# Performance work log

Measured on AMD Instinct MI355X. Metric: run time of the kernel, lower is better.

Reference implementation:

```python
import jax, jax.numpy as jnp
import numpy as np

# ---- module hyperparameters ----
B, L, F = 128, 720, 128
SEG = 24            # segment_length
NSEG = L // SEG     # 30 input segments
WIN = 15            # window_size
NPRED = 96 // SEG   # 4 prediction segments
D = 128             # encode_dim
H = 512             # hidden_dim
DECAY = 0.9
C = 1.0             # curvature
EPS = 1e-6
MAXN = 1.0 - 1e-5   # max radius of Poincare ball (c=1)
SQC = 1.0           # sqrt(C)

# ---- Poincare-ball manifold ops ----
def _sqnorm(x):
    return jnp.sum(x * x, axis=-1, keepdims=True)

def _norm(x):
    return jnp.sqrt(jnp.maximum(_sqnorm(x), EPS * EPS))

def _project(x):
    n = _norm(x)
    return jnp.where(n > MAXN, x * (MAXN / n), x)

def _artanh(x):
    return jnp.arctanh(jnp.clip(x, -1.0 + 1e-7, 1.0 - 1e-7))

def mobius_add(x, y):
    xy = jnp.sum(x * y, axis=-1, keepdims=True)
    x2, y2 = _sqnorm(x), _sqnorm(y)
    num = (1.0 + 2.0 * C * xy + C * y2) * x + (1.0 - C * x2) * y
    den = 1.0 + 2.0 * C * xy + C * C * x2 * y2
    return num / jnp.maximum(den, EPS)

def expmap0(v):
    n = _norm(v)
    return _project(jnp.tanh(SQC * n) * v / (SQC * n))

def logmap0(y):
    n = _norm(y)
    return _artanh(SQC * n) * y / (SQC * n)

def expmap(x, v):
    lam = 2.0 / jnp.maximum(1.0 - C * _sqnorm(x), EPS)
    n = _norm(v)
    second = jnp.tanh(SQC * lam * n / 2.0) * v / (SQC * n)
    return _project(mobius_add(x, second))

def logmap(x, y):
    d = mobius_add(-x, y)
    n = _norm(d)
    lam = 2.0 / jnp.maximum(1.0 - C * _sqnorm(x), EPS)
    return (2.0 / (SQC * lam)) * _artanh(SQC * n) * d / n


def setup_inputs() -> dict:
    key = jax.random.key(0)
    ks = jax.random.split(key, 12)
    s = 0.05
    return {
        'trend':           0.5 * jax.random.normal(ks[0], (B, L, F), jnp.float32),
        'seasonal_coarse': 0.5 * jax.random.normal(ks[1], (B, L, F), jnp.float32),
        'seasonal_fine':   0.5 * jax.random.normal(ks[2], (B, L, F), jnp.float32),
        'residual':        0.5 * jax.random.normal(ks[3], (B, L, F), jnp.float32),
        'W_t': s * jax.random.normal(ks[4], (SEG, D), jnp.float32), 'b_t': jnp.zeros((D,), jnp.float32),
        'W_c': s * jax.random.normal(ks[5], (SEG, D), jnp.float32), 'b_c': jnp.zeros((D,), jnp.float32),
        'W_f': s * jax.random.normal(ks[6], (SEG, D), jnp.float32), 'b_f': jnp.zeros((D,), jnp.float32),
        'W_r': s * jax.random.normal(ks[7], (SEG, D), jnp.float32), 'b_r': jnp.zeros((D,), jnp.float32),
        'alpha': jnp.array([0.5], jnp.float32),
        'W1': s * jax.random.normal(ks[8], (D, H), jnp.float32), 'b1': jnp.zeros((H,), jnp.float32),
        'W2': s * jax.random.normal(ks[9], (H, SEG), jnp.float32), 'b2': jnp.zeros((SEG,), jnp.float32),
    }


def reference(trend, seasonal_coarse, seasonal_fine, residual,
              W_t, b_t, W_c, b_c, W_f, b_f, W_r, b_r,
              alpha, W1, b1, W2, b2):
    b, l, f = trend.shape

    def collapse(x):  # [B,L,F] -> [B*F, NSEG, SEG]
        return x.transpose(0, 2, 1).reshape(b * f, NSEG, SEG)

    t_s, c_s, f_s, r_s = map(collapse, (trend, seasonal_coarse, seasonal_fine, residual))

    # per-segment tangent encoding (channel-independent, shared params)
    tan = (jnp.einsum('bns,sd->bnd', t_s, W_t) + b_t
           + jnp.einsum('bns,sd->bnd', c_s, W_c) + b_c
           + jnp.einsum('bns,sd->bnd', f_s, W_f) + b_f
           + jnp.einsum('bns,sd->bnd', r_s, W_r) + b_r)
    z = expmap0(tan)                     # [BF, NSEG, D] on the ball
    z_cur = z[:, -WIN:, :]

    idx = jnp.arange(WIN - 1, dtype=jnp.float32)
    w = DECAY ** (WIN - 2 - idx)
    w = w / w.sum()

    preds, latents = [], []
    for _ in range(NPRED):
        z_last = z_cur[:, -1]
        vel = logmap(z_cur[:, :-1], z_cur[:, 1:])
        avg_v = jnp.sum(vel * w[None, :, None], axis=1)    # [BF, D]
        z_next = expmap(z_last, alpha * avg_v)             # dynamics step
        latents.append(z_next)
        # reconstruction head: logmap0 -> MLP -> segment
        t0 = logmap0(z_next)
        seg = jax.nn.relu(t0 @ W1 + b1) @ W2 + b2          # [BF, SEG]
        preds.append(seg)
        z_cur = jnp.concatenate([z_cur[:, 1:], z_next[:, None]], axis=1)

    p = jnp.stack(preds, axis=1).reshape(b * f, NPRED * SEG)
    predictions = p.reshape(b, f, NPRED * SEG).transpose(0, 2, 1)  # [B, pred_len, F]
    return predictions
```

## Files before the change

### kernel.cpp

```cpp
#include <hip/hip_runtime.h>
#include <hip/hip_bf16.h>

namespace {
constexpr int kL = 720, kF = 128;
constexpr int kWin = 15;
constexpr float kEps = 1e-6f;
constexpr float kMaxN = 1.0f - 1e-5f;
constexpr int kT0off = 360;
constexpr int ZTR = 132;
constexpr int AROW = 104;
constexpr size_t kOffT0   = 0;
constexpr size_t kOffW1   = 16777216;
constexpr size_t kOffW2   = kOffW1 + 131072;
constexpr size_t kOffBt   = kOffW2 + 32768;
constexpr size_t kOffBsum = kOffBt + 73728;
constexpr size_t kOffHid  = 17825792;
constexpr size_t kWsSplit = kOffHid + 67108864;
}

typedef float f32x4 __attribute__((ext_vector_type(4)));
typedef short s16x8 __attribute__((ext_vector_type(8)));

__device__ __forceinline__ float rcp_f(float x) { return __builtin_amdgcn_rcpf(x); }
__device__ __forceinline__ float sqrt_f(float x) { return __builtin_amdgcn_sqrtf(x); }
__device__ __forceinline__ float tanh_f(float x) {
  float t = __builtin_amdgcn_exp2f(x * -2.8853900817779268f);
  return (1.0f - t) * rcp_f(1.0f + t);
}
__device__ __forceinline__ float artanh_f(float n) {
  float nc = fminf(n, 1.0f - 1e-7f);
  return 0.34657359027997264f * __builtin_amdgcn_logf((1.0f + nc) * rcp_f(1.0f - nc));
}

template<int CTRL>
__device__ __forceinline__ float dpp_add(float v) {
  int mv = __builtin_amdgcn_update_dpp(0, __float_as_int(v), CTRL, 0xF, 0xF, false);
  return v + __int_as_float(mv);
}
__device__ __forceinline__ float sum16(float v) {
  v = dpp_add<0xB1>(v);
  v = dpp_add<0x4E>(v);
  v = dpp_add<0x141>(v);
  v = dpp_add<0x128>(v);
  return v;
}
__device__ __forceinline__ float sum64(float v) {
  v = sum16(v);
  v += __shfl_xor(v, 16);
  v += __shfl_xor(v, 32);
  return v;
}
__device__ __forceinline__ float rlane(float v, int i) {
  return __int_as_float(__builtin_amdgcn_readlane(__float_as_int(v), i));
}

extern "C" __global__ __launch_bounds__(256)
void mwhf_prep(const float* __restrict__ W1, const float* __restrict__ W2,
               const float* __restrict__ W_t, const float* __restrict__ W_c,
               const float* __restrict__ W_f, const float* __restrict__ W_r,
               const float* __restrict__ b_t, const float* __restrict__ b_c,
               const float* __restrict__ b_f, const float* __restrict__ b_r,
               __hip_bfloat16* __restrict__ W1bf, __hip_bfloat16* __restrict__ W2bf,
               __hip_bfloat16* __restrict__ BtH, __hip_bfloat16* __restrict__ BtM,
               __hip_bfloat16* __restrict__ BtL, float* __restrict__ bsum)
{
  const int b = blockIdx.x, tid = threadIdx.x;
  if (b < 64) {
    const int n0 = b * 8;
    for (int e = tid; e < 1024; e += 256) {
      int n_l = e & 7, k = e >> 3;
      W1bf[(size_t)(n0 + n_l) * 128 + k] = __float2bfloat16(W1[(size_t)k * 512 + n0 + n_l]);
    }
  } else if (b < 68) {
    const int k0 = (b - 64) * 128;
    for (int e = tid; e < 4096; e += 256) {
      int p = e >> 7, k_l = e & 127;
      float v = (p < 24) ? W2[(size_t)(k0 + k_l) * 24 + p] : 0.0f;
      W2bf[(size_t)p * 512 + k0 + k_l] = __float2bfloat16(v);
    }
  } else if (b < 72) {
    const int st = b - 68;
    const float* src = (st == 0) ? W_t : (st == 1) ? W_c : (st == 2) ? W_f : W_r;
    for (int e = tid; e < 3072; e += 256) {
      int s = e >> 7, d = e & 127;
      float x = src[e];
      __hip_bfloat16 h = __float2bfloat16(x);
      float r1 = x - __bfloat162float(h);
      __hip_bfloat16 m = __float2bfloat16(r1);
      float r2 = r1 - __bfloat162float(m);
      const int o = d * 96 + st * 24 + s;
      BtH[o] = h;
      BtM[o] = m;
      BtL[o] = __float2bfloat16(r2);
    }
  } else {
    if (tid < 128) bsum[tid] = b_t[tid] + b_c[tid] + b_f[tid] + b_r[tid];
  }
}

extern "C" __global__ __launch_bounds__(256, 4)
void mwhf_k1(const float* __restrict__ trend,
             const float* __restrict__ seas_c,
             const float* __restrict__ seas_f,
             const float* __restrict__ resid,
             const __hip_bfloat16* __restrict__ BtH,
             const __hip_bfloat16* __restrict__ BtM,
             const __hip_bfloat16* __restrict__ BtL,
             const float* __restrict__ bsum,
             const float* __restrict__ alpha,
             __hip_bfloat16* __restrict__ t0_out)
{
  __shared__ __align__(16) char smem_raw[3 * 64 * AROW * 2];
  __shared__ float z2s[80];
  __shared__ float pds[80];

  float* ublk = (float*)smem_raw;
  __hip_bfloat16* Ah = (__hip_bfloat16*)smem_raw;
  __hip_bfloat16* Am = Ah + 64 * AROW;
  __hip_bfloat16* Al = Am + 64 * AROW;

  const int tid = threadIdx.x;
  const int bix = blockIdx.x;
  const int bb = (bix & 7) * 16 + (bix >> 8);
  const int f0 = ((bix >> 3) & 31) * 4;
  const int row0 = bb * 128 + f0;

  for (int e = tid; e < 192; e += 256) {
    int rr = e / 48, cc = e - rr * 48;
    int off = (rr * 16 + 15) * AROW;
    ((unsigned int*)(Ah + off))[cc] = 0u;
    ((unsigned int*)(Am + off))[cc] = 0u;
    ((unsigned int*)(Al + off))[cc] = 0u;
  }
  {
    const float* ptrs[4] = {trend, seas_c, seas_f, resid};
    for (int e = tid; e < 1440; e += 256) {
      int seg = e / 96;
      int k = e - seg * 96;
      int st = k / 24, s = k - st * 24;
      const float* p = ptrs[st];
      float4 v = *(const float4*)&p[(size_t)(bb * kL + kT0off + seg * 24 + s) * kF + f0];
      float xv[4] = {v.x, v.y, v.z, v.w};
#pragma unroll
      for (int f = 0; f < 4; ++f) {
        int m = f * 16 + seg;
        __hip_bfloat16 h = __float2bfloat16(xv[f]);
        float r1 = xv[f] - __bfloat162float(h);
        __hip_bfloat16 mm = __float2bfloat16(r1);
        float r2 = r1 - __bfloat162float(mm);
        Ah[m * AROW + k] = h;
        Am[m * AROW + k] = mm;
        Al[m * AROW + k] = __float2bfloat16(r2);
      }
    }
  }
  __syncthreads();

  const int w = tid >> 6;
  const int lane = tid & 63;
  const int l16 = lane & 15, quad = lane >> 4;

  f32x4 acc0[8];
  float scale4[4], zz4[4];
  {
    s16x8 ah[3], am[3], al[3];
    const int abase = (w * 16 + l16) * AROW + quad * 8;
#pragma unroll
    for (int ks = 0; ks < 3; ++ks) {
      ah[ks] = *(const s16x8*)(Ah + abase + ks * 32);
      am[ks] = *(const s16x8*)(Am + abase + ks * 32);
      al[ks] = *(const s16x8*)(Al + abase + ks * 32);
    }
#pragma unroll
    for (int t = 0; t < 8; ++t) acc0[t] = (f32x4)0.f;
    const __hip_bfloat16* bhp = BtH + l16 * 96 + quad * 8;
    const __hip_bfloat16* bmp = BtM + l16 * 96 + quad * 8;
    const __hip_bfloat16* blp = BtL + l16 * 96 + quad * 8;
#pragma unroll
    for (int t = 0; t < 8; ++t) {
#pragma unroll
      for (int ks = 0; ks < 3; ++ks) {
        s16x8 bh = *(const s16x8*)(bhp + t * 1536 + ks * 32);
        s16x8 bm = *(const s16x8*)(bmp + t * 1536 + ks * 32);
        s16x8 bl = *(const s16x8*)(blp + t * 1536 + ks * 32);
        acc0[t] = __builtin_amdgcn_mfma_f32_16x16x32_bf16(ah[ks], bh, acc0[t], 0, 0, 0);
        acc0[t] = __builtin_amdgcn_mfma_f32_16x16x32_bf16(am[ks], bh, acc0[t], 0, 0, 0);
        acc0[t] = __builtin_amdgcn_mfma_f32_16x16x32_bf16(ah[ks], bm, acc0[t], 0, 0, 0);
        acc0[t] = __builtin_amdgcn_mfma_f32_16x16x32_bf16(al[ks], bh, acc0[t], 0, 0, 0);
        acc0[t] = __builtin_amdgcn_mfma_f32_16x16x32_bf16(ah[ks], bl, acc0[t], 0, 0, 0);
        acc0[t] = __builtin_amdgcn_mfma_f32_16x16x32_bf16(am[ks], bm, acc0[t], 0, 0, 0);
      }
    }
    float part[4] = {0.f, 0.f, 0.f, 0.f};
#pragma unroll
    for (int t = 0; t < 8; ++t) {
      float bv = bsum[t * 16 + l16];
#pragma unroll
      for (int r = 0; r < 4; ++r) {
        float v = acc0[t][r] + bv;
        acc0[t][r] = v;
        part[r] += v * v;
      }
    }
#pragma unroll
    for (int r = 0; r < 4; ++r) part[r] = sum16(part[r]);
#pragma unroll
    for (int r = 0; r < 4; ++r) {
      float v2 = part[r];
      float nv = sqrt_f(fmaxf(v2, 1e-12f));
      float sc = tanh_f(nv) * rcp_f(nv);
      float y2 = sc * sc * v2;
      float yn = sqrt_f(fmaxf(y2, 1e-12f));
      float proj = (yn > kMaxN) ? (kMaxN * rcp_f(yn)) : 1.0f;
      scale4[r] = sc * proj;
      zz4[r] = y2 * proj * proj;
    }
  }
  __syncthreads();
  {
#pragma unroll
    for (int r = 0; r < 4; ++r) {
      int row = quad * 4 + r;
      if (row < kWin) {
#pragma unroll
        for (int t = 0; t < 8; ++t)
          ublk[(w * kWin + row) * ZTR + t * 16 + l16] = acc0[t][r] * scale4[r];
        if (l16 == 0) z2s[w * 20 + row] = zz4[r];
      }
    }
  }
  __syncthreads();

  {
    const int l = lane;
    float zx[19], zy[19];
#pragma unroll
    for (int j = 0; j < 15; ++j) {
      float2 v = *(const float2*)&ublk[(w * kWin + j) * ZTR + 2 * l];
      zx[j] = v.x; zy[j] = v.y;
    }
    {
      float pd[14];
#pragma unroll
      for (int j = 0; j < 14; ++j) pd[j] = zx[j] * zx[j + 1] + zy[j] * zy[j + 1];
#pragma unroll
      for (int j = 0; j < 14; ++j) pd[j] = sum64(pd[j]);
      if (l == 0) {
#pragma unroll
        for (int j = 0; j < 14; ++j) pds[w * 20 + j] = pd[j];
      }
    }

    const float alp = alpha[0];
    const float cw14 = (l < 14)
        ? __builtin_amdgcn_exp2f((float)(13 - l) * -0.15200309344504997f) * 0.12966260f
        : 0.f;

#pragma unroll
    for (int it = 0; it < 4; ++it) {
      float cA = 0.f, cB = 0.f, cW = 0.f;
      if (l < 14) {
        float dp = pds[w * 20 + it + l];
        float x2 = z2s[w * 20 + it + l];
        float y2 = z2s[w * 20 + it + l + 1];
        cA = 1.f - 2.f * dp + y2;
        cB = 1.f - x2;
        float den = fmaxf(1.f - 2.f * dp + x2 * y2, kEps);
        float invd = rcp_f(den);
        float d2 = (cA * cA * x2 - 2.f * cA * cB * dp + cB * cB * y2) * (invd * invd);
        float n = sqrt_f(fmaxf(d2, 1e-12f));
        float coef = fmaxf(cB, kEps) * artanh_f(n) * rcp_f(n);
        cW = cw14 * coef * invd;
      }
      float avx = 0.f, avy = 0.f;
#pragma unroll
      for (int i = 0; i < 14; ++i) {
        float sA = rlane(cA, i), sB = rlane(cB, i), sW = rlane(cW, i);
        float tx = sB * zx[it + i + 1] - sA * zx[it + i];
        float ty = sB * zy[it + i + 1] - sA * zy[it + i];
        avx += sW * tx;
        avy += sW * ty;
      }
      float vx = alp * avx, vy = alp * avy;
      const int pl = it + 14;
      float x2l = z2s[w * 20 + pl];
      float v2 = vx * vx + vy * vy;
      float xdv = zx[pl] * vx + zy[pl] * vy;
      v2 = sum64(v2);
      xdv = sum64(xdv);
      float nv = sqrt_f(fmaxf(v2, 1e-12f));
      float lam = 2.f * rcp_f(fmaxf(1.f - x2l, kEps));
      float co = tanh_f(0.5f * lam * nv) * rcp_f(nv);
      float s2 = co * co * v2;
      float xy = co * xdv;
      float P = 1.f + 2.f * xy + s2;
      float Q = 1.f - x2l;
      float den2 = fmaxf(1.f + 2.f * xy + x2l * s2, kEps);
      float invd2 = rcp_f(den2);
      float znx = (P * zx[pl] + Q * co * vx) * invd2;
      float zny = (P * zy[pl] + Q * co * vy) * invd2;
      float zn2 = (P * P * x2l + 2.f * P * Q * xy + Q * Q * s2) * (invd2 * invd2);
      float pdn = (P * x2l + Q * xy) * invd2;
      float yn = sqrt_f(fmaxf(zn2, 1e-12f));
      float proj = (yn > kMaxN) ? (kMaxN * rcp_f(yn)) : 1.f;
      znx *= proj; zny *= proj;
      zn2 *= proj * proj;
      pdn *= proj;
      zx[15 + it] = znx; zy[15 + it] = zny;
      if (l == 0) {
        z2s[w * 20 + 15 + it] = zn2;
        pds[w * 20 + 14 + it] = pdn;
      }
      float n0 = sqrt_f(fmaxf(zn2, 1e-12f));
      float fac = artanh_f(n0) * rcp_f(n0);
      __hip_bfloat162 hv;
      hv.x = __float2bfloat16(fac * znx);
      hv.y = __float2bfloat16(fac * zny);
      *(__hip_bfloat162*)(t0_out + ((size_t)(row0 + w) * 4 + it) * 128 + 2 * l) = hv;
    }
  }
}

extern "C" __global__ __launch_bounds__(256, 4)
void mwhf_k2a(const __hip_bfloat16* __restrict__ t0g,
              const __hip_bfloat16* __restrict__ W1bf,
              const float* __restrict__ b1,
              __hip_bfloat16* __restrict__ hid)
{
  const int tid = threadIdx.x;
  const int w = tid >> 6, lane = tid & 63;
  const int l16 = lane & 15, quad = lane >> 4;
  const int mbase = blockIdx.x * 32;
  const int ng = w * 128;

  s16x8 afr[2][4];
#pragma unroll
  for (int s = 0; s < 2; ++s)
#pragma unroll
    for (int kc = 0; kc < 4; ++kc)
      afr[s][kc] = *(const s16x8*)(t0g + (size_t)(mbase + s * 16 + l16) * 128 + kc * 32 + quad * 8);

  f32x4 acc[2][8];
#pragma unroll
  for (int s = 0; s < 2; ++s)
#pragma unroll
    for (int t = 0; t < 8; ++t) acc[s][t] = (f32x4)0.f;

#pragma unroll
  for (int t = 0; t < 8; ++t) {
    const __hip_bfloat16* bp = W1bf + (size_t)(ng + t * 16 + l16) * 128 + quad * 8;
#pragma unroll
    for (int kc = 0; kc < 4; ++kc) {
      s16x8 bfr = *(const s16x8*)(bp + kc * 32);
      acc[0][t] = __builtin_amdgcn_mfma_f32_16x16x32_bf16(afr[0][kc], bfr, acc[0][t], 0, 0, 0);
      acc[1][t] = __builtin_amdgcn_mfma_f32_16x16x32_bf16(afr[1][kc], bfr, acc[1][t], 0, 0, 0);
    }
  }
#pragma unroll
  for (int t = 0; t < 8; ++t) {
    const int n = ng + t * 16 + l16;
    float bv = b1[n];
#pragma unroll
    for (int s = 0; s < 2; ++s)
#pragma unroll
      for (int r = 0; r < 4; ++r) {
        int m = mbase + s * 16 + quad * 4 + r;
        float h = fmaxf(acc[s][t][r] + bv, 0.f);
        hid[(size_t)m * 512 + n] = __float2bfloat16(h);
      }
  }
}

extern "C" __global__ __launch_bounds__(256, 4)
void mwhf_k2b(const __hip_bfloat16* __restrict__ hid,
              const __hip_bfloat16* __restrict__ W2bf,
              const float* __restrict__ b2,
              float* __restrict__ outp)
{
  const int tid = threadIdx.x;
  const int w = tid >> 6, lane = tid & 63;
  const int l16 = lane & 15, quad = lane >> 4;
  const int mb = (blockIdx.x * 4 + w) * 32;

  f32x4 acc[2][2];
#pragma unroll
  for (int s = 0; s < 2; ++s)
#pragma unroll
    for (int t = 0; t < 2; ++t) acc[s][t] = (f32x4)0.f;

#pragma unroll 4
  for (int kc = 0; kc < 16; ++kc) {
    s16x8 a0 = *(const s16x8*)(hid + (size_t)(mb + l16) * 512 + kc * 32 + quad * 8);
    s16x8 a1 = *(const s16x8*)(hid + (size_t)(mb + 16 + l16) * 512 + kc * 32 + quad * 8);
#pragma unroll
    for (int t = 0; t < 2; ++t) {
      s16x8 bfr = *(const s16x8*)(W2bf + (size_t)(t * 16 + l16) * 512 + kc * 32 + quad * 8);
      acc[0][t] = __builtin_amdgcn_mfma_f32_16x16x32_bf16(a0, bfr, acc[0][t], 0, 0, 0);
      acc[1][t] = __builtin_amdgcn_mfma_f32_16x16x32_bf16(a1, bfr, acc[1][t], 0, 0, 0);
    }
  }
#pragma unroll
  for (int t = 0; t < 2; ++t) {
    const int p = t * 16 + l16;
    if (p < 24) {
      float bv = b2[p];
#pragma unroll
      for (int s = 0; s < 2; ++s)
#pragma unroll
        for (int r = 0; r < 4; ++r) {
          int m = mb + s * 16 + quad * 4 + r;
          int bbi = m >> 9, it = m & 3, f = (m >> 2) & 127;
          outp[(size_t)bbi * 12288 + (it * 24 + p) * 128 + f] = acc[s][t][r] + bv;
        }
    }
  }
}

extern "C" __global__ __launch_bounds__(256)
void mwhf_k2f(const __hip_bfloat16* __restrict__ t0g,
              const __hip_bfloat16* __restrict__ W1bf,
              const __hip_bfloat16* __restrict__ W2bf,
              const float* __restrict__ b1, const float* __restrict__ b2,
              float* __restrict__ outp)
{
  __shared__ __align__(16) char smem[147456];
  s16x8* Av   = (s16x8*)smem;
  s16x8* W1v  = (s16x8*)(smem + 16384);
  s16x8* W2v  = (s16x8*)(smem + 16384);
  float* red  = (float*)(smem + 49152);
  __hip_bfloat16* hid = (__hip_bfloat16*)(smem + 81920);
  s16x8* hidv = (s16x8*)(smem + 81920);

  const int tid = threadIdx.x;
  const int m0 = blockIdx.x * 64;
  const int w = tid >> 6, lane = tid & 63;
  const int l16 = lane & 15, quad = lane >> 4;

  {
    const s16x8* src = (const s16x8*)(t0g + (size_t)m0 * 128);
    for (int e = tid; e < 1024; e += 256) {
      int m = e >> 4, c = e & 15;
      Av[m * 16 + (c ^ (m & 7))] = src[e];
    }
  }
  f32x4 acc[4][4];
  for (int nh = 0; nh < 2; ++nh) {
    __syncthreads();
    {
      const s16x8* src = (const s16x8*)W1bf + (size_t)nh * 4096;
      for (int e = tid; e < 4096; e += 256) {
        int n = e >> 4, c = e & 15;
        W1v[n * 16 + (c ^ (n & 7))] = src[e];
      }
    }
    __syncthreads();
#pragma unroll
    for (int s = 0; s < 4; ++s)
#pragma unroll
      for (int t = 0; t < 4; ++t) acc[s][t] = (f32x4)0.f;
#pragma unroll
    for (int ks = 0; ks < 4; ++ks) {
      s16x8 a[4];
#pragma unroll
      for (int s = 0; s < 4; ++s)
        a[s] = Av[(s * 16 + l16) * 16 + ((ks * 4 + quad) ^ (l16 & 7))];
#pragma unroll
      for (int t = 0; t < 4; ++t) {
        int nl = w * 64 + t * 16 + l16;
        s16x8 bfr = W1v[nl * 16 + ((ks * 4 + quad) ^ (nl & 7))];
#pragma unroll
        for (int s = 0; s < 4; ++s)
          acc[s][t] = __builtin_amdgcn_mfma_f32_16x16x32_bf16(a[s], bfr, acc[s][t], 0, 0, 0);
      }
    }
#pragma unroll
    for (int t = 0; t < 4; ++t) {
      int nabs = nh * 256 + w * 64 + t * 16 + l16;
      float bv = b1[nabs];
#pragma unroll
      for (int s = 0; s < 4; ++s)
#pragma unroll
        for (int r = 0; r < 4; ++r) {
          int m = s * 16 + quad * 4 + r;
          float h = fmaxf(acc[s][t][r] + bv, 0.f);
          hid[m * 512 + (nabs ^ ((m & 7) << 3))] = __float2bfloat16(h);
        }
    }
  }
  __syncthreads();
  {
    const s16x8* src = (const s16x8*)W2bf;
    for (int e = tid; e < 2048; e += 256) {
      int p = e >> 6, c = e & 63;
      W2v[p * 64 + (c ^ (p & 7))] = src[e];
    }
  }
  __syncthreads();
  {
    f32x4 a2[2];
    a2[0] = (f32x4)0.f; a2[1] = (f32x4)0.f;
    const int m = w * 16 + l16;
#pragma unroll 4
    for (int ks = 0; ks < 16; ++ks) {
      s16x8 av = hidv[m * 64 + ((ks * 4 + quad) ^ (l16 & 7))];
#pragma unroll
      for (int t = 0; t < 2; ++t) {
        s16x8 bfr = W2v[(t * 16 + l16) * 64 + ((ks * 4 + quad) ^ (l16 & 7))];
        a2[t] = __builtin_amdgcn_mfma_f32_16x16x32_bf16(av, bfr, a2[t], 0, 0, 0);
      }
    }
#pragma unroll
    for (int t = 0; t < 2; ++t)
#pragma unroll
      for (int r = 0; r < 4; ++r) {
        int p = t * 16 + l16;
        if (p < 24) red[(w * 16 + quad * 4 + r) * 25 + p] = a2[t][r];
      }
  }
  __syncthreads();
  {
    const int bbi = m0 >> 9;
    const int f0 = (m0 >> 2) & 127;
    for (int e = tid; e < 1536; e += 256) {
      int fi = e & 15;
      int rest = e >> 4;
      int p = rest % 24;
      int it = rest / 24;
      outp[(size_t)bbi * 12288 + rest * 128 + f0 + fi] = red[(fi * 4 + it) * 25 + p] + b2[p];
    }
  }
}

extern "C" void kernel_launch(void* const* d_in, const int* in_sizes, int n_in,
                              void* d_out, int out_size, void* d_ws, size_t ws_size,
                              hipStream_t stream) {
  (void)in_sizes; (void)n_in; (void)out_size;
  const float* trend = (const float*)d_in[0];
  const float* sc    = (const float*)d_in[1];
  const float* sf    = (const float*)d_in[2];
  const float* rs    = (const float*)d_in[3];
  const float* W_t   = (const float*)d_in[4];
  const float* b_t   = (const float*)d_in[5];
  const float* W_c   = (const float*)d_in[6];
  const float* b_c   = (const float*)d_in[7];
  const float* W_f   = (const float*)d_in[8];
  const float* b_f   = (const float*)d_in[9];
  const float* W_r   = (const float*)d_in[10];
  const float* b_r   = (const float*)d_in[11];
  const float* alpha = (const float*)d_in[12];
  const float* W1    = (const float*)d_in[13];
  const float* b1    = (const float*)d_in[14];
  const float* W2    = (const float*)d_in[15];
  const float* b2    = (const float*)d_in[16];

  char* ws = (char*)d_ws;
  __hip_bfloat16* t0   = (__hip_bfloat16*)(ws + kOffT0);
  __hip_bfloat16* W1bf = (__hip_bfloat16*)(ws + kOffW1);
  __hip_bfloat16* W2bf = (__hip_bfloat16*)(ws + kOffW2);
  __hip_bfloat16* BtH  = (__hip_bfloat16*)(ws + kOffBt);
  __hip_bfloat16* BtM  = BtH + 12288;
  __hip_bfloat16* BtL  = BtM + 12288;
  float* bsum = (float*)(ws + kOffBsum);
  __hip_bfloat16* hid = (__hip_bfloat16*)(ws + kOffHid);
  float* outp = (float*)d_out;

  hipLaunchKernelGGL(mwhf_prep, dim3(73), dim3(256), 0, stream,
                     W1, W2, W_t, W_c, W_f, W_r, b_t, b_c, b_f, b_r,
                     W1bf, W2bf, BtH, BtM, BtL, bsum);
  hipLaunchKernelGGL(mwhf_k1, dim3(4096), dim3(256), 0, stream,
                     trend, sc, sf, rs, BtH, BtM, BtL, bsum, alpha, t0);
  if (ws_size >= kWsSplit) {
    hipLaunchKernelGGL(mwhf_k2a, dim3(2048), dim3(256), 0, stream, t0, W1bf, b1, hid);
    hipLaunchKernelGGL(mwhf_k2b, dim3(512), dim3(256), 0, stream, hid, W2bf, b2, outp);
  } else {
    hipLaunchKernelGGL(mwhf_k2f, dim3(1024), dim3(256), 0, stream,
                       t0, W1bf, W2bf, b1, b2, outp);
  }
}
```

Before: 387.3 us.

## Split segment encoder and dynamics into separate kernels via workspace latents

Splits the fused encoder+dynamics kernel into two kernels. The first runs the three-way bf16-split MFMA encode and expmap0, then writes the 15 window latents and their squared norms to global workspace. The second reads them back and runs the 4-step Poincaré dynamics to produce t0. The aim is to let each kernel use fewer registers and less shared memory and so run at higher occupancy, at the cost of about 120MB of extra global write and read traffic and one more launch. The first kernel also splits A into bf16 parts in registers instead of staging three bf16 copies in shared memory.

```diff
diff --git a/kernel.cpp b/kernel.cpp
--- a/kernel.cpp
+++ b/kernel.cpp
@@ -9,13 +9,17 @@
 constexpr int kT0off = 360;
 constexpr int ZTR = 132;
 constexpr int AROW = 104;
+constexpr int AFR = 100;
 constexpr size_t kOffT0   = 0;
 constexpr size_t kOffW1   = 16777216;
 constexpr size_t kOffW2   = kOffW1 + 131072;
 constexpr size_t kOffBt   = kOffW2 + 32768;
 constexpr size_t kOffBsum = kOffBt + 73728;
+constexpr size_t kOffZ2   = 17018880;
 constexpr size_t kOffHid  = 17825792;
+constexpr size_t kOffZ    = 18874368;
 constexpr size_t kWsSplit = kOffHid + 67108864;
+constexpr size_t kWsNew   = kOffZ + 125829120;
 }
 
 typedef float f32x4 __attribute__((ext_vector_type(4)));
@@ -52,6 +56,12 @@
 }
 __device__ __forceinline__ float rlane(float v, int i) {
   return __int_as_float(__builtin_amdgcn_readlane(__float_as_int(v), i));
+}
+__device__ __forceinline__ unsigned short rne_bf16(float f, float& fval) {
+  unsigned u = __float_as_uint(f);
+  unsigned r = (u + 0x7FFFu + ((u >> 16) & 1u)) & 0xFFFF0000u;
+  fval = __uint_as_float(r);
+  return (unsigned short)(r >> 16);
 }
 
 extern "C" __global__ __launch_bounds__(256)
@@ -99,6 +109,222 @@
 }
 
 extern "C" __global__ __launch_bounds__(256, 4)
+void mwhf_k1a(const float* __restrict__ trend,
+              const float* __restrict__ seas_c,
+              const float* __restrict__ seas_f,
+              const float* __restrict__ resid,
+              const __hip_bfloat16* __restrict__ BtH,
+              const __hip_bfloat16* __restrict__ BtM,
+              const __hip_bfloat16* __restrict__ BtL,
+              const float* __restrict__ bsum,
+              float* __restrict__ z_ws, float* __restrict__ z2_ws)
+{
+  __shared__ __align__(16) float Af[64 * AFR];
+
+  const int tid = threadIdx.x;
+  const int bix = blockIdx.x;
+  const int bb = (bix & 7) * 16 + (bix >> 8);
+  const int f0 = ((bix >> 3) & 31) * 4;
+  const int row0 = bb * 128 + f0;
+
+  for (int e = tid; e < 384; e += 256) {
+    int rr = e / 96, cc = e - rr * 96;
+    Af[(rr * 16 + 15) * AFR + cc] = 0.f;
+  }
+  {
+    const float* ptrs[4] = {trend, seas_c, seas_f, resid};
+    for (int e = tid; e < 1440; e += 256) {
+      int seg = e / 96, k = e - seg * 96;
+      int st = k / 24, s = k - st * 24;
+      float4 v = *(const float4*)&ptrs[st][(size_t)(bb * kL + kT0off + seg * 24 + s) * kF + f0];
+      Af[(0 * 16 + seg) * AFR + k] = v.x;
+      Af[(1 * 16 + seg) * AFR + k] = v.y;
+      Af[(2 * 16 + seg) * AFR + k] = v.z;
+      Af[(3 * 16 + seg) * AFR + k] = v.w;
+    }
+  }
+  __syncthreads();
+
+  const int w = tid >> 6, lane = tid & 63;
+  const int l16 = lane & 15, quad = lane >> 4;
+
+  s16x8 ah[3], am[3], al[3];
+  {
+    const float* ar = &Af[(w * 16 + l16) * AFR + quad * 8];
+#pragma unroll
+    for (int ks = 0; ks < 3; ++ks) {
+#pragma unroll
+      for (int j = 0; j < 8; ++j) {
+        float x = ar[ks * 32 + j];
+        unsigned hu = __float_as_uint(x) & 0xFFFF0000u;
+        float r1 = x - __uint_as_float(hu);
+        float mf; unsigned short mb = rne_bf16(r1, mf);
+        float r2 = r1 - mf;
+        float lf; unsigned short lb = rne_bf16(r2, lf);
+        (void)lf;
+        ah[ks][j] = (short)(hu >> 16);
+        am[ks][j] = (short)mb;
+        al[ks][j] = (short)lb;
+      }
+    }
+  }
+
+  f32x4 acc0[8];
+#pragma unroll
+  for (int t = 0; t < 8; ++t) acc0[t] = (f32x4)0.f;
+  const __hip_bfloat16* bhp = BtH + l16 * 96 + quad * 8;
+  const __hip_bfloat16* bmp = BtM + l16 * 96 + quad * 8;
+  const __hip_bfloat16* blp = BtL + l16 * 96 + quad * 8;
+#pragma unroll
+  for (int t = 0; t < 8; ++t) {
+#pragma unroll
+    for (int ks = 0; ks < 3; ++ks) {
+      s16x8 bh = *(const s16x8*)(bhp + t * 1536 + ks * 32);
+      s16x8 bm = *(const s16x8*)(bmp + t * 1536 + ks * 32);
+      s16x8 bl = *(const s16x8*)(blp + t * 1536 + ks * 32);
+      acc0[t] = __builtin_amdgcn_mfma_f32_16x16x32_bf16(ah[ks], bh, acc0[t], 0, 0, 0);
+      acc0[t] = __builtin_amdgcn_mfma_f32_16x16x32_bf16(am[ks], bh, acc0[t], 0, 0, 0);
+      acc0[t] = __builtin_amdgcn_mfma_f32_16x16x32_bf16(ah[ks], bm, acc0[t], 0, 0, 0);
+      acc0[t] = __builtin_amdgcn_mfma_f32_16x16x32_bf16(al[ks], bh, acc0[t], 0, 0, 0);
+      acc0[t] = __builtin_amdgcn_mfma_f32_16x16x32_bf16(ah[ks], bl, acc0[t], 0, 0, 0);
+      acc0[t] = __builtin_amdgcn_mfma_f32_16x16x32_bf16(am[ks], bm, acc0[t], 0, 0, 0);
+    }
+  }
+  float part[4] = {0.f, 0.f, 0.f, 0.f};
+#pragma unroll
+  for (int t = 0; t < 8; ++t) {
+    float bv = bsum[t * 16 + l16];
+#pragma unroll
+    for (int r = 0; r < 4; ++r) {
+      float v = acc0[t][r] + bv;
+      acc0[t][r] = v;
+      part[r] += v * v;
+    }
+  }
+#pragma unroll
+  for (int r = 0; r < 4; ++r) part[r] = sum16(part[r]);
+  const int ro = row0 + w;
+#pragma unroll
+  for (int r = 0; r < 4; ++r) {
+    const int seg = quad * 4 + r;
+    float v2 = part[r];
+    float nv = sqrt_f(fmaxf(v2, 1e-12f));
+    float sc = tanh_f(nv) * rcp_f(nv);
+    float y2 = sc * sc * v2;
+    float yn = sqrt_f(fmaxf(y2, 1e-12f));
+    float proj = (yn > kMaxN) ? (kMaxN * rcp_f(yn)) : 1.0f;
+    float scl = sc * proj;
+    if (seg < kWin) {
+#pragma unroll
+      for (int t = 0; t < 8; ++t)
+        z_ws[(size_t)ro * 1920 + seg * 128 + t * 16 + l16] = acc0[t][r] * scl;
+      if (l16 == 0) z2_ws[ro * 16 + seg] = y2 * proj * proj;
+    }
+  }
+}
+
+extern "C" __global__ __launch_bounds__(256, 6)
+void mwhf_k1b(const float* __restrict__ z_ws, const float* __restrict__ z2_ws,
+              const float* __restrict__ alpha,
+              __hip_bfloat16* __restrict__ t0_out)
+{
+  __shared__ float z2s[80];
+  __shared__ float pds[80];
+  const int tid = threadIdx.x;
+  const int w = tid >> 6, l = tid & 63;
+  const int ro = blockIdx.x * 4 + w;
+
+  float zx[19], zy[19];
+  const float* zr = z_ws + (size_t)ro * 1920;
+#pragma unroll
+  for (int j = 0; j < 15; ++j) {
+    float2 v = *(const float2*)&zr[j * 128 + 2 * l];
+    zx[j] = v.x; zy[j] = v.y;
+  }
+  if (l < 15) z2s[w * 20 + l] = z2_ws[ro * 16 + l];
+
+  {
+    float pd[14];
+#pragma unroll
+    for (int j = 0; j < 14; ++j) pd[j] = zx[j] * zx[j + 1] + zy[j] * zy[j + 1];
+#pragma unroll
+    for (int j = 0; j < 14; ++j) pd[j] = sum64(pd[j]);
+    if (l == 0) {
+#pragma unroll
+      for (int j = 0; j < 14; ++j) pds[w * 20 + j] = pd[j];
+    }
+  }
+
+  const float alp = alpha[0];
+  const float cw14 = (l < 14)
+      ? __builtin_amdgcn_exp2f((float)(13 - l) * -0.15200309344504997f) * 0.12966260f
+      : 0.f;
+
+#pragma unroll
+  for (int it = 0; it < 4; ++it) {
+    float cA = 0.f, cB = 0.f, cW = 0.f;
+    if (l < 14) {
+      float dp = pds[w * 20 + it + l];
+      float x2 = z2s[w * 20 + it + l];
+      float y2 = z2s[w * 20 + it + l + 1];
+      cA = 1.f - 2.f * dp + y2;
+      cB = 1.f - x2;
+      float den = fmaxf(1.f - 2.f * dp + x2 * y2, kEps);
+      float invd = rcp_f(den);
+      float d2 = (cA * cA * x2 - 2.f * cA * cB * dp + cB * cB * y2) * (invd * invd);
+      float n = sqrt_f(fmaxf(d2, 1e-12f));
+      float coef = fmaxf(cB, kEps) * artanh_f(n) * rcp_f(n);
+      cW = cw14 * coef * invd;
+    }
+    float avx = 0.f, avy = 0.f;
+#pragma unroll
+    for (int i = 0; i < 14; ++i) {
+      float sA = rlane(cA, i), sB = rlane(cB, i), sW = rlane(cW, i);
+      float tx = sB * zx[it + i + 1] - sA * zx[it + i];
+      float ty = sB * zy[it + i + 1] - sA * zy[it + i];
+      avx += sW * tx;
+      avy += sW * ty;
+    }
+    float vx = alp * avx, vy = alp * avy;
+    const int pl = it + 14;
+    float x2l = z2s[w * 20 + pl];
+    float v2 = vx * vx + vy * vy;
+    float xdv = zx[pl] * vx + zy[pl] * vy;
+    v2 = sum64(v2);
+    xdv = sum64(xdv);
+    float nv = sqrt_f(fmaxf(v2, 1e-12f));
+    float lam = 2.f * rcp_f(fmaxf(1.f - x2l, kEps));
+    float co = tanh_f(0.5f * lam * nv) * rcp_f(nv);
+    float s2 = co * co * v2;
+    float xy = co * xdv;
+    float P = 1.f + 2.f * xy + s2;
+    float Q = 1.f - x2l;
+    float den2 = fmaxf(1.f + 2.f * xy + x2l * s2, kEps);
+    float invd2 = rcp_f(den2);
+    float znx = (P * zx[pl] + Q * co * vx) * invd2;
+    float zny = (P * zy[pl] + Q * co * vy) * invd2;
+    float zn2 = (P * P * x2l + 2.f * P * Q * xy + Q * Q * s2) * (invd2 * invd2);
+    float pdn = (P * x2l + Q * xy) * invd2;
+    float yn = sqrt_f(fmaxf(zn2, 1e-12f));
+    float proj = (yn > kMaxN) ? (kMaxN * rcp_f(yn)) : 1.f;
+    znx *= proj; zny *= proj;
+    zn2 *= proj * proj;
+    pdn *= proj;
+    zx[15 + it] = znx; zy[15 + it] = zny;
+    if (l == 0) {
+      z2s[w * 20 + 15 + it] = zn2;
+      pds[w * 20 + 14 + it] = pdn;
+    }
+    float n0 = sqrt_f(fmaxf(zn2, 1e-12f));
+    float fac = artanh_f(n0) * rcp_f(n0);
+    __hip_bfloat162 hv;
+    hv.x = __float2bfloat16(fac * znx);
+    hv.y = __float2bfloat16(fac * zny);
+    *(__hip_bfloat162*)(t0_out + ((size_t)ro * 4 + it) * 128 + 2 * l) = hv;
+  }
+}
+
+extern "C" __global__ __launch_bounds__(256, 4)
 void mwhf_k1(const float* __restrict__ trend,
              const float* __restrict__ seas_c,
              const float* __restrict__ seas_f,
@@ -250,12 +476,10 @@
         for (int j = 0; j < 14; ++j) pds[w * 20 + j] = pd[j];
       }
     }
-
     const float alp = alpha[0];
     const float cw14 = (l < 14)
         ? __builtin_amdgcn_exp2f((float)(13 - l) * -0.15200309344504997f) * 0.12966260f
         : 0.f;
-
 #pragma unroll
     for (int it = 0; it < 4; ++it) {
       float cA = 0.f, cB = 0.f, cW = 0.f;
@@ -561,14 +785,23 @@
   __hip_bfloat16* BtM  = BtH + 12288;
   __hip_bfloat16* BtL  = BtM + 12288;
   float* bsum = (float*)(ws + kOffBsum);
+  float* z2w  = (float*)(ws + kOffZ2);
+  float* zw   = (float*)(ws + kOffZ);
   __hip_bfloat16* hid = (__hip_bfloat16*)(ws + kOffHid);
   float* outp = (float*)d_out;
 
   hipLaunchKernelGGL(mwhf_prep, dim3(73), dim3(256), 0, stream,
                      W1, W2, W_t, W_c, W_f, W_r, b_t, b_c, b_f, b_r,
                      W1bf, W2bf, BtH, BtM, BtL, bsum);
-  hipLaunchKernelGGL(mwhf_k1, dim3(4096), dim3(256), 0, stream,
-                     trend, sc, sf, rs, BtH, BtM, BtL, bsum, alpha, t0);
+  if (ws_size >= kWsNew) {
+    hipLaunchKernelGGL(mwhf_k1a, dim3(4096), dim3(256), 0, stream,
+                       trend, sc, sf, rs, BtH, BtM, BtL, bsum, zw, z2w);
+    hipLaunchKernelGGL(mwhf_k1b, dim3(4096), dim3(256), 0, stream,
+                       zw, z2w, alpha, t0);
+  } else {
+    hipLaunchKernelGGL(mwhf_k1, dim3(4096), dim3(256), 0, stream,
+                       trend, sc, sf, rs, BtH, BtM, BtL, bsum, alpha, t0);
+  }
   if (ws_size >= kWsSplit) {
     hipLaunchKernelGGL(mwhf_k2a, dim3(2048), dim3(256), 0, stream, t0, W1bf, b1, hid);
     hipLaunchKernelGGL(mwhf_k2b, dim3(512), dim3(256), 0, stream, hid, W2bf, b2, outp);
```

Result: slower. 405.5 us (+4.7%).

## Fuse MLP hidden and output GEMMs through shared memory, dropping global hidden buffer

Applied to the files above, without the earlier changes.

Merges the two-kernel MLP head into one kernel that keeps the ReLU hidden activations of each 32-row tile in swizzled shared memory and immediately runs the second GEMM. This removes the round trip of a large bf16 hidden tensor through global memory and one kernel launch. In exchange, each block uses 32 KB of LDS, which may limit occupancy, and the second GEMM has only a little MFMA work per wave. The old fallback fused kernel and the workspace-size branch are removed.

```diff
diff --git a/kernel.cpp b/kernel.cpp
--- a/kernel.cpp
+++ b/kernel.cpp
@@ -14,8 +14,6 @@
 constexpr size_t kOffW2   = kOffW1 + 131072;
 constexpr size_t kOffBt   = kOffW2 + 32768;
 constexpr size_t kOffBsum = kOffBt + 73728;
-constexpr size_t kOffHid  = 17825792;
-constexpr size_t kWsSplit = kOffHid + 67108864;
 }
 
 typedef float f32x4 __attribute__((ext_vector_type(4)));
@@ -250,12 +248,10 @@
         for (int j = 0; j < 14; ++j) pds[w * 20 + j] = pd[j];
       }
     }
-
     const float alp = alpha[0];
     const float cw14 = (l < 14)
         ? __builtin_amdgcn_exp2f((float)(13 - l) * -0.15200309344504997f) * 0.12966260f
         : 0.f;
-
 #pragma unroll
     for (int it = 0; it < 4; ++it) {
       float cA = 0.f, cB = 0.f, cW = 0.f;
@@ -322,11 +318,15 @@
 }
 
 extern "C" __global__ __launch_bounds__(256, 4)
-void mwhf_k2a(const __hip_bfloat16* __restrict__ t0g,
+void mwhf_k2g(const __hip_bfloat16* __restrict__ t0g,
               const __hip_bfloat16* __restrict__ W1bf,
-              const float* __restrict__ b1,
-              __hip_bfloat16* __restrict__ hid)
+              const __hip_bfloat16* __restrict__ W2bf,
+              const float* __restrict__ b1, const float* __restrict__ b2,
+              float* __restrict__ outp)
 {
+  __shared__ __align__(16) __hip_bfloat16 hids[32 * 512];
+  s16x8* hidv = (s16x8*)hids;
+
   const int tid = threadIdx.x;
   const int w = tid >> 6, lane = tid & 63;
   const int l16 = lane & 15, quad = lane >> 4;
@@ -358,175 +358,38 @@
   }
 #pragma unroll
   for (int t = 0; t < 8; ++t) {
-    const int n = ng + t * 16 + l16;
-    float bv = b1[n];
+    const int nl = ng + t * 16 + l16;
+    float bv = b1[nl];
 #pragma unroll
     for (int s = 0; s < 2; ++s)
 #pragma unroll
       for (int r = 0; r < 4; ++r) {
-        int m = mbase + s * 16 + quad * 4 + r;
+        int m = s * 16 + quad * 4 + r;
         float h = fmaxf(acc[s][t][r] + bv, 0.f);
-        hid[(size_t)m * 512 + n] = __float2bfloat16(h);
-      }
-  }
-}
-
-extern "C" __global__ __launch_bounds__(256, 4)
-void mwhf_k2b(const __hip_bfloat16* __restrict__ hid,
-              const __hip_bfloat16* __restrict__ W2bf,
-              const float* __restrict__ b2,
-              float* __restrict__ outp)
-{
-  const int tid = threadIdx.x;
-  const int w = tid >> 6, lane = tid & 63;
-  const int l16 = lane & 15, quad = lane >> 4;
-  const int mb = (blockIdx.x * 4 + w) * 32;
-
-  f32x4 acc[2][2];
-#pragma unroll
-  for (int s = 0; s < 2; ++s)
-#pragma unroll
-    for (int t = 0; t < 2; ++t) acc[s][t] = (f32x4)0.f;
-
+        hids[m * 512 + (nl ^ ((m & 7) << 3))] = __float2bfloat16(h);
+      }
+  }
+  __syncthreads();
+
+  {
+    const int s2i = w & 1, t2 = w >> 1;
+    f32x4 a2 = (f32x4)0.f;
+    const int mrow = s2i * 16 + l16;
 #pragma unroll 4
-  for (int kc = 0; kc < 16; ++kc) {
-    s16x8 a0 = *(const s16x8*)(hid + (size_t)(mb + l16) * 512 + kc * 32 + quad * 8);
-    s16x8 a1 = *(const s16x8*)(hid + (size_t)(mb + 16 + l16) * 512 + kc * 32 + quad * 8);
-#pragma unroll
-    for (int t = 0; t < 2; ++t) {
-      s16x8 bfr = *(const s16x8*)(W2bf + (size_t)(t * 16 + l16) * 512 + kc * 32 + quad * 8);
-      acc[0][t] = __builtin_amdgcn_mfma_f32_16x16x32_bf16(a0, bfr, acc[0][t], 0, 0, 0);
-      acc[1][t] = __builtin_amdgcn_mfma_f32_16x16x32_bf16(a1, bfr, acc[1][t], 0, 0, 0);
-    }
-  }
-#pragma unroll
-  for (int t = 0; t < 2; ++t) {
-    const int p = t * 16 + l16;
+    for (int kc = 0; kc < 16; ++kc) {
+      s16x8 av = hidv[mrow * 64 + ((kc * 4 + quad) ^ (l16 & 7))];
+      s16x8 bfr = *(const s16x8*)(W2bf + (size_t)(t2 * 16 + l16) * 512 + kc * 32 + quad * 8);
+      a2 = __builtin_amdgcn_mfma_f32_16x16x32_bf16(av, bfr, a2, 0, 0, 0);
+    }
+    const int p = t2 * 16 + l16;
     if (p < 24) {
       float bv = b2[p];
 #pragma unroll
-      for (int s = 0; s < 2; ++s)
-#pragma unroll
-        for (int r = 0; r < 4; ++r) {
-          int m = mb + s * 16 + quad * 4 + r;
-          int bbi = m >> 9, it = m & 3, f = (m >> 2) & 127;
-          outp[(size_t)bbi * 12288 + (it * 24 + p) * 128 + f] = acc[s][t][r] + bv;
-        }
-    }
-  }
-}
-
-extern "C" __global__ __launch_bounds__(256)
-void mwhf_k2f(const __hip_bfloat16* __restrict__ t0g,
-              const __hip_bfloat16* __restrict__ W1bf,
-              const __hip_bfloat16* __restrict__ W2bf,
-              const float* __restrict__ b1, const float* __restrict__ b2,
-              float* __restrict__ outp)
-{
-  __shared__ __align__(16) char smem[147456];
-  s16x8* Av   = (s16x8*)smem;
-  s16x8* W1v  = (s16x8*)(smem + 16384);
-  s16x8* W2v  = (s16x8*)(smem + 16384);
-  float* red  = (float*)(smem + 49152);
-  __hip_bfloat16* hid = (__hip_bfloat16*)(smem + 81920);
-  s16x8* hidv = (s16x8*)(smem + 81920);
-
-  const int tid = threadIdx.x;
-  const int m0 = blockIdx.x * 64;
-  const int w = tid >> 6, lane = tid & 63;
-  const int l16 = lane & 15, quad = lane >> 4;
-
-  {
-    const s16x8* src = (const s16x8*)(t0g + (size_t)m0 * 128);
-    for (int e = tid; e < 1024; e += 256) {
-      int m = e >> 4, c = e & 15;
-      Av[m * 16 + (c ^ (m & 7))] = src[e];
-    }
-  }
-  f32x4 acc[4][4];
-  for (int nh = 0; nh < 2; ++nh) {
-    __syncthreads();
-    {
-      const s16x8* src = (const s16x8*)W1bf + (size_t)nh * 4096;
-      for (int e = tid; e < 4096; e += 256) {
-        int n = e >> 4, c = e & 15;
-        W1v[n * 16 + (c ^ (n & 7))] = src[e];
-      }
-    }
-    __syncthreads();
-#pragma unroll
-    for (int s = 0; s < 4; ++s)
-#pragma unroll
-      for (int t = 0; t < 4; ++t) acc[s][t] = (f32x4)0.f;
-#pragma unroll
-    for (int ks = 0; ks < 4; ++ks) {
-      s16x8 a[4];
-#pragma unroll
-      for (int s = 0; s < 4; ++s)
-        a[s] = Av[(s * 16 + l16) * 16 + ((ks * 4 + quad) ^ (l16 & 7))];
-#pragma unroll
-      for (int t = 0; t < 4; ++t) {
-        int nl = w * 64 + t * 16 + l16;
-        s16x8 bfr = W1v[nl * 16 + ((ks * 4 + quad) ^ (nl & 7))];
-#pragma unroll
-        for (int s = 0; s < 4; ++s)
-          acc[s][t] = __builtin_amdgcn_mfma_f32_16x16x32_bf16(a[s], bfr, acc[s][t], 0, 0, 0);
-      }
-    }
-#pragma unroll
-    for (int t = 0; t < 4; ++t) {
-      int nabs = nh * 256 + w * 64 + t * 16 + l16;
-      float bv = b1[nabs];
-#pragma unroll
-      for (int s = 0; s < 4; ++s)
-#pragma unroll
-        for (int r = 0; r < 4; ++r) {
-          int m = s * 16 + quad * 4 + r;
-          float h = fmaxf(acc[s][t][r] + bv, 0.f);
-          hid[m * 512 + (nabs ^ ((m & 7) << 3))] = __float2bfloat16(h);
-        }
-    }
-  }
-  __syncthreads();
-  {
-    const s16x8* src = (const s16x8*)W2bf;
-    for (int e = tid; e < 2048; e += 256) {
-      int p = e >> 6, c = e & 63;
-      W2v[p * 64 + (c ^ (p & 7))] = src[e];
-    }
-  }
-  __syncthreads();
-  {
-    f32x4 a2[2];
-    a2[0] = (f32x4)0.f; a2[1] = (f32x4)0.f;
-    const int m = w * 16 + l16;
-#pragma unroll 4
-    for (int ks = 0; ks < 16; ++ks) {
-      s16x8 av = hidv[m * 64 + ((ks * 4 + quad) ^ (l16 & 7))];
-#pragma unroll
-      for (int t = 0; t < 2; ++t) {
-        s16x8 bfr = W2v[(t * 16 + l16) * 64 + ((ks * 4 + quad) ^ (l16 & 7))];
-        a2[t] = __builtin_amdgcn_mfma_f32_16x16x32_bf16(av, bfr, a2[t], 0, 0, 0);
-      }
-    }
-#pragma unroll
-    for (int t = 0; t < 2; ++t)
-#pragma unroll
       for (int r = 0; r < 4; ++r) {
-        int p = t * 16 + l16;
-        if (p < 24) red[(w * 16 + quad * 4 + r) * 25 + p] = a2[t][r];
-      }
-  }
-  __syncthreads();
-  {
-    const int bbi = m0 >> 9;
-    const int f0 = (m0 >> 2) & 127;
-    for (int e = tid; e < 1536; e += 256) {
-      int fi = e & 15;
-      int rest = e >> 4;
-      int p = rest % 24;
-      int it = rest / 24;
-      outp[(size_t)bbi * 12288 + rest * 128 + f0 + fi] = red[(fi * 4 + it) * 25 + p] + b2[p];
+        int m = mbase + s2i * 16 + quad * 4 + r;
+        int bbi = m >> 9, it = m & 3, f = (m >> 2) & 127;
+        outp[(size_t)bbi * 12288 + (it * 24 + p) * 128 + f] = a2[r] + bv;
+      }
     }
   }
 }
@@ -534,7 +397,7 @@
 extern "C" void kernel_launch(void* const* d_in, const int* in_sizes, int n_in,
                               void* d_out, int out_size, void* d_ws, size_t ws_size,
                               hipStream_t stream) {
-  (void)in_sizes; (void)n_in; (void)out_size;
+  (void)in_sizes; (void)n_in; (void)out_size; (void)ws_size;
   const float* trend = (const float*)d_in[0];
   const float* sc    = (const float*)d_in[1];
   const float* sf    = (const float*)d_in[2];
@@ -561,7 +424,6 @@
   __hip_bfloat16* BtM  = BtH + 12288;
   __hip_bfloat16* BtL  = BtM + 12288;
   float* bsum = (float*)(ws + kOffBsum);
-  __hip_bfloat16* hid = (__hip_bfloat16*)(ws + kOffHid);
   float* outp = (float*)d_out;
 
   hipLaunchKernelGGL(mwhf_prep, dim3(73), dim3(256), 0, stream,
@@ -569,11 +431,6 @@
                      W1bf, W2bf, BtH, BtM, BtL, bsum);
   hipLaunchKernelGGL(mwhf_k1, dim3(4096), dim3(256), 0, stream,
                      trend, sc, sf, rs, BtH, BtM, BtL, bsum, alpha, t0);
-  if (ws_size >= kWsSplit) {
-    hipLaunchKernelGGL(mwhf_k2a, dim3(2048), dim3(256), 0, stream, t0, W1bf, b1, hid);
-    hipLaunchKernelGGL(mwhf_k2b, dim3(512), dim3(256), 0, stream, hid, W2bf, b2, outp);
-  } else {
-    hipLaunchKernelGGL(mwhf_k2f, dim3(1024), dim3(256), 0, stream,
-                       t0, W1bf, W2bf, b1, b2, outp);
-  }
-}
+  hipLaunchKernelGGL(mwhf_k2g, dim3(2048), dim3(256), 0, stream,
+                     t0, W1bf, W2bf, b1, b2, outp);
+}
```

New measurement: 365.3 us. -5.7%, faster.
